# Kernel tuning notes

Measured on AMD Instinct MI355X. Metric: run time of the kernel, lower is better.

Reference implementation:

```python
import jax, jax.numpy as jnp
import numpy as np

C = 768            # config.channels
CH, CW = 16, 16    # coarse span shape for group 'screen'
N = CH * CW        # total coarse positions = 256
FH, FW, FP = 16, 16, 2
F = FH * FW * FP   # fine_total = 512
K = 4              # top4 sample mode
B = 1024           # sb


def _ln(x, g, b, eps=1e-5):
    m = jnp.mean(x, axis=-1, keepdims=True)
    v = jnp.mean((x - m) ** 2, axis=-1, keepdims=True)
    return (x - m) / jnp.sqrt(v + eps) * g + b


def _mlp3(x, W1, b1, W2, b2, W3, b3):
    h = jax.nn.gelu(x @ W1 + b1)
    h = jax.nn.gelu(h @ W2 + b2)
    return h @ W3 + b3


def setup_inputs() -> dict:
    key = jax.random.key(0)
    ks = jax.random.split(key, 16)

    def w(k, fan_in, shape):
        return jax.random.normal(k, shape, jnp.float32) * (1.0 / np.sqrt(fan_in))

    return {
        "x": jax.random.normal(ks[0], (B, C), jnp.float32),
        "g_in": jnp.ones((C,), jnp.float32),
        "b_in": jnp.zeros((C,), jnp.float32),
        # coarse head: C -> C -> C -> N
        "cW1": w(ks[1], C, (C, C)), "cb1": jnp.zeros((C,), jnp.float32),
        "cW2": w(ks[2], C, (C, C)), "cb2": jnp.zeros((C,), jnp.float32),
        "cW3": w(ks[3], C, (C, N)), "cb3": jnp.zeros((N,), jnp.float32),
        # coarse embedding
        "emb": jax.random.normal(ks[4], (N, C), jnp.float32),
        "g_e": jnp.ones((C,), jnp.float32),
        "b_e": jnp.zeros((C,), jnp.float32),
        # fine head: 2C -> C -> C -> F
        "fW1": w(ks[5], 2 * C, (2 * C, C)), "fb1": jnp.zeros((C,), jnp.float32),
        "fW2": w(ks[6], C, (C, C)), "fb2": jnp.zeros((C,), jnp.float32),
        "fW3": w(ks[7], C, (C, F)), "fb3": jnp.zeros((F,), jnp.float32),
        # no-op head
        "nW": w(ks[8], C, (C, 1)), "nb": jnp.zeros((1,), jnp.float32),
    }


def reference(x, g_in, b_in, cW1, cb1, cW2, cb2, cW3, cb3, emb, g_e, b_e,
              fW1, fb1, fW2, fb2, fW3, fb3, nW, nb):
    b = x.shape[0]
    xn = _ln(x, g_in, b_in)                                   # (b, C)
    no_op = xn @ nW + nb                                      # (b, 1)
    coarse = _mlp3(xn, cW1, cb1, cW2, cb2, cW3, cb3)          # (b, N)

    # top4 routing
    _, i = jax.lax.top_k(coarse, K)                           # (b, K) int32
    e = _ln(emb[i], g_e, b_e)                                 # (b, K, C)
    fine_in = jnp.concatenate(
        [jnp.broadcast_to(xn[:, None, :], (b, K, C)), e], axis=-1)  # (b, K, 2C)
    fine = _mlp3(fine_in, fW1, fb1, fW2, fb2, fW3, fb3)       # (b, K, F)

    log_f = jnp.log(jnp.float32(F))
    xfull = jnp.broadcast_to(coarse[:, :, None], (b, N, F)) - log_f  # (b, N, F)
    upd = fine + log_f - jax.nn.logsumexp(fine, axis=-1, keepdims=True)
    xfull = xfull.at[jnp.arange(b)[:, None], i].add(upd)      # scatter-combine

    # per-group permute: (b, ch, cw, fh, fw, fp) -> (b, ch, fh, cw, fw, fp)
    xg = xfull.reshape(b, CH, CW, FH, FW, FP)
    xg = jnp.transpose(xg, (0, 1, 3, 2, 4, 5)).reshape(b, -1)
    return jnp.concatenate([no_op, xg], axis=-1)              # (b, 1 + N*F)
```

## Files before the change

### kernel.cpp

```cpp
#include <hip/hip_runtime.h>
#include <hip/hip_bf16.h>
#include <math.h>

typedef unsigned short u16;
typedef unsigned int   u32;
typedef __attribute__((ext_vector_type(8))) short s16x8;
typedef __attribute__((ext_vector_type(4))) float f32x4;

#define CB 768
#define NB 256
#define FB 512
#define BATCH 1024
#define OUTC 131073
#define LOGF 6.2383246250395077f

__device__ __forceinline__ u16 f2bf(float f){
    u32 u = __float_as_uint(f);
    u32 r = u + 0x7FFFu + ((u >> 16) & 1u);
    return (u16)(r >> 16);
}
__device__ __forceinline__ float bf2f(u16 s){ return __uint_as_float(((u32)s) << 16); }
__device__ __forceinline__ bool probe_bf(const void* g){ return ((const u16*)g)[0] == 0x3F80u; }
__device__ __forceinline__ float loadraw(const void* p, size_t i, bool isbf){
    return isbf ? bf2f(((const u16*)p)[i]) : ((const float*)p)[i];
}
__device__ __forceinline__ void split3(float f, u16& h, u16& l, u16& q){
    h = f2bf(f); float r1 = f - bf2f(h);
    l = f2bf(r1); float r2 = r1 - bf2f(l);
    q = f2bf(r2);
}
__device__ __forceinline__ float gelu_f(float x){
    return 0.5f * x * (1.0f + tanhf(0.7978845608028654f * (x + 0.044715f * x * x * x)));
}
__device__ __forceinline__ f32x4 mfma16x16x32(s16x8 a, s16x8 b, f32x4 c){
    return __builtin_amdgcn_mfma_f32_16x16x32_bf16(a, b, c, 0, 0, 0);
}

__device__ __forceinline__ float blockReduce(float v, float* sb, bool domax){
    #pragma unroll
    for (int o = 32; o > 0; o >>= 1){
        float ov = __shfl_down(v, o, 64);
        v = domax ? fmaxf(v, ov) : (v + ov);
    }
    int w = threadIdx.x >> 6, lane = threadIdx.x & 63;
    if (lane == 0) sb[w] = v;
    __syncthreads();
    float r = domax ? fmaxf(fmaxf(sb[0], sb[1]), fmaxf(sb[2], sb[3]))
                    : (sb[0] + sb[1] + sb[2] + sb[3]);
    __syncthreads();
    return r;
}

struct TransDesc { const void* src; u16* dh; u16* dl; int K; int N; int start; int tilesX; };
struct TD6 { TransDesc d[6]; };

#define T_TRANS   3456
#define T_LNX_END 4480
#define T_LEM_END 4736
#define T_CI_END  4752
#define T_KS_END  4768
#define T_GRID    4769

__global__ __launch_bounds__(256) void prep_k(TD6 td,
        const void* x, const void* g, const void* bb, const void* nW, const void* nb,
        const void* emb, const void* ge, const void* be, const void* cb3, const void* ginp,
        u16* __restrict__ xh, u16* __restrict__ xl, u16* __restrict__ xq,
        u16* __restrict__ lnemb, float* __restrict__ noop,
        float* __restrict__ coarse, unsigned char* __restrict__ ksel,
        float* __restrict__ sumexp){
    __shared__ float t[32][33];
    __shared__ float sb[4];
    bool isbf = probe_bf(ginp);
    int blk = blockIdx.x, tid = threadIdx.x;
    if (blk < T_TRANS){
        int e = 0;
        #pragma unroll
        for (int i = 1; i < 6; i++) if (blk >= td.d[i].start) e = i;
        TransDesc d = td.d[e];
        int rel = blk - d.start;
        int n0 = (rel % d.tilesX) * 32;
        int k0 = (rel / d.tilesX) * 32;
        int tx = tid & 31, ty = tid >> 5;
        #pragma unroll
        for (int i = 0; i < 32; i += 8)
            t[ty + i][tx] = loadraw(d.src, (size_t)(k0 + ty + i) * d.N + n0 + tx, isbf);
        __syncthreads();
        #pragma unroll
        for (int i = 0; i < 32; i += 8){
            float f = t[tx][ty + i];
            u16 h = f2bf(f);
            d.dh[(size_t)(n0 + ty + i) * d.K + k0 + tx] = h;
            if (d.dl)
                d.dl[(size_t)(n0 + ty + i) * d.K + k0 + tx] = f2bf(f - bf2f(h));
        }
    } else if (blk < T_LNX_END){
        int b = blk - T_TRANS;
        float v[3];
        #pragma unroll
        for (int i = 0; i < 3; i++) v[i] = loadraw(x, (size_t)b * CB + tid + i * 256, isbf);
        float mean = blockReduce(v[0] + v[1] + v[2], sb, false) * (1.0f / 768.0f);
        float d0 = v[0] - mean, d1 = v[1] - mean, d2 = v[2] - mean;
        float var = blockReduce(d0*d0 + d1*d1 + d2*d2, sb, false) * (1.0f / 768.0f);
        float inv = 1.0f / sqrtf(var + 1e-5f);
        float dot = 0.0f;
        #pragma unroll
        for (int i = 0; i < 3; i++){
            int c = tid + i * 256;
            float xi = (v[i] - mean) * inv * loadraw(g, c, isbf) + loadraw(bb, c, isbf);
            u16 h, l, q; split3(xi, h, l, q);
            size_t o = (size_t)b * CB + c;
            xh[o] = h; xl[o] = l; xq[o] = q;
            dot += xi * loadraw(nW, c, isbf);
        }
        dot = blockReduce(dot, sb, false);
        if (tid == 0) noop[b] = dot + loadraw(nb, 0, isbf);
    } else if (blk < T_LEM_END){
        int n = blk - T_LNX_END;
        float v[3];
        #pragma unroll
        for (int i = 0; i < 3; i++) v[i] = loadraw(emb, (size_t)n * CB + tid + i * 256, isbf);
        float mean = blockReduce(v[0] + v[1] + v[2], sb, false) * (1.0f / 768.0f);
        float d0 = v[0] - mean, d1 = v[1] - mean, d2 = v[2] - mean;
        float var = blockReduce(d0*d0 + d1*d1 + d2*d2, sb, false) * (1.0f / 768.0f);
        float inv = 1.0f / sqrtf(var + 1e-5f);
        #pragma unroll
        for (int i = 0; i < 3; i++){
            int c = tid + i * 256;
            lnemb[(size_t)n * CB + c] =
                f2bf((v[i] - mean) * inv * loadraw(ge, c, isbf) + loadraw(be, c, isbf));
        }
    } else if (blk < T_CI_END){
        int base = (blk - T_LEM_END) * 16384;
        #pragma unroll
        for (int j = 0; j < 64; j++){
            int i = base + j * 256 + tid;
            coarse[i] = loadraw(cb3, i & 255, isbf);
        }
    } else if (blk < T_KS_END){
        int base = (blk - T_CI_END) * 4096;
        u32* kp = (u32*)ksel;
        #pragma unroll
        for (int j = 0; j < 16; j++) kp[base + j * 256 + tid] = 0xFFFFFFFFu;
    } else {
        #pragma unroll
        for (int j = 0; j < 16; j++) sumexp[j * 256 + tid] = 0.0f;
    }
}

template<int ASPLIT, int BSPLIT, int ACT, int OUTMODE, int TM, int TN, int GATHER>
__device__ __forceinline__ void gemm_body(u16* sm,
        const u16* __restrict__ Ah, const u16* __restrict__ Al, const u16* __restrict__ Aq,
        const int* __restrict__ gidx,
        const u16* __restrict__ Bth, const u16* __restrict__ Btl,
        const void* __restrict__ bias, bool isbf,
        void* __restrict__ o0, void* __restrict__ o1, void* __restrict__ o2,
        int bx, int by, int kbeg, int kend, int N, int lda, int ldb){
    constexpr int LDA = 72;
    constexpr int MT = TM / 32;
    constexpr int NT = TN / 64;
    constexpr int AC = TM / 64;
    constexpr int BC = TN / 64;
    u16* As = sm;
    u16* Bs = sm + ASPLIT * TM * LDA;
    const int m0 = by * TM, n0 = bx * TN;
    const int tid = threadIdx.x;
    const int w = tid >> 6, lane = tid & 63, lm = lane & 15, q = lane >> 4;
    const int wr = w & 1, wc = w >> 1;
    f32x4 acc[MT][NT];
    #pragma unroll
    for (int i = 0; i < MT; i++)
        #pragma unroll
        for (int j = 0; j < NT; j++) acc[i][j] = (f32x4)(0.0f);
    const int ar = (AC == 2) ? (tid >> 2) : (tid >> 3);
    const int ac = (AC == 2) ? ((tid & 3) * 16) : ((tid & 7) * 8);
    const int bn = (BC == 2) ? (tid >> 2) : (tid >> 3);
    const int bc = (BC == 2) ? ((tid & 3) * 16) : ((tid & 7) * 8);
    const u16* Apl[3] = { Ah, Al, Aq };
    const u16* Bpl[2] = { Bth, Btl };
    const int arow = GATHER ? gidx[m0 + ar] : (m0 + ar);

    s16x8 pa[ASPLIT][AC], pb[BSPLIT][BC];
    auto load_regs = [&](int kk){
        #pragma unroll
        for (int s = 0; s < ASPLIT; s++){
            const u16* sp = Apl[s] + (size_t)arow * lda + kk + ac;
            pa[s][0] = *(const s16x8*)(sp);
            if (AC == 2) pa[s][1] = *(const s16x8*)(sp + 8);
        }
        #pragma unroll
        for (int s = 0; s < BSPLIT; s++){
            const u16* sp = Bpl[s] + (size_t)(n0 + bn) * ldb + kk + bc;
            pb[s][0] = *(const s16x8*)(sp);
            if (BC == 2) pb[s][1] = *(const s16x8*)(sp + 8);
        }
    };

    load_regs(kbeg);
    for (int k0 = kbeg; k0 < kend; k0 += 64){
        __syncthreads();
        #pragma unroll
        for (int s = 0; s < ASPLIT; s++){
            *(s16x8*)&As[s*TM*LDA + ar*LDA + ac] = pa[s][0];
            if (AC == 2) *(s16x8*)&As[s*TM*LDA + ar*LDA + ac + 8] = pa[s][1];
        }
        #pragma unroll
        for (int s = 0; s < BSPLIT; s++){
            *(s16x8*)&Bs[s*TN*LDA + bn*LDA + bc] = pb[s][0];
            if (BC == 2) *(s16x8*)&Bs[s*TN*LDA + bn*LDA + bc + 8] = pb[s][1];
        }
        __syncthreads();
        if (k0 + 64 < kend) load_regs(k0 + 64);

        #pragma unroll
        for (int kk = 0; kk < 2; kk++){
            s16x8 afr[ASPLIT][MT], bfr[BSPLIT][NT];
            #pragma unroll
            for (int mt = 0; mt < MT; mt++)
                #pragma unroll
                for (int s = 0; s < ASPLIT; s++)
                    afr[s][mt] = *(const s16x8*)&As[s*TM*LDA + ((mt*2 + wr)*16 + lm)*LDA + kk*32 + q*8];
            #pragma unroll
            for (int nt = 0; nt < NT; nt++)
                #pragma unroll
                for (int s = 0; s < BSPLIT; s++)
                    bfr[s][nt] = *(const s16x8*)&Bs[s*TN*LDA + ((nt*4 + wc)*16 + lm)*LDA + kk*32 + q*8];
            #pragma unroll
            for (int mt = 0; mt < MT; mt++)
                #pragma unroll
                for (int nt = 0; nt < NT; nt++){
                    acc[mt][nt] = mfma16x16x32(afr[0][mt], bfr[0][nt], acc[mt][nt]);
                    if (ASPLIT == 3){
                        acc[mt][nt] = mfma16x16x32(afr[1][mt], bfr[0][nt], acc[mt][nt]);
                        acc[mt][nt] = mfma16x16x32(afr[2][mt], bfr[0][nt], acc[mt][nt]);
                    }
                    if (BSPLIT == 2){
                        acc[mt][nt] = mfma16x16x32(afr[0][mt], bfr[1][nt], acc[mt][nt]);
                        if (ASPLIT == 3)
                            acc[mt][nt] = mfma16x16x32(afr[1][mt], bfr[1][nt], acc[mt][nt]);
                    }
                }
        }
    }

    if (OUTMODE == 3){
        #pragma unroll
        for (int nt = 0; nt < NT; nt++){
            int n = n0 + (nt*4 + wc)*16 + lm;
            #pragma unroll
            for (int mt = 0; mt < MT; mt++)
                #pragma unroll
                for (int r = 0; r < 4; r++){
                    int m = m0 + (mt*2 + wr)*16 + q*4 + r;
                    atomicAdd(&((float*)o0)[(size_t)m * N + n], acc[mt][nt][r]);
                }
        }
    } else if (OUTMODE == 4){
        #pragma unroll
        for (int mt = 0; mt < MT; mt++)
            #pragma unroll
            for (int r = 0; r < 4; r++){
                int m = m0 + (mt*2 + wr)*16 + q*4 + r;
                float esum = 0.0f;
                #pragma unroll
                for (int nt = 0; nt < NT; nt++){
                    int n = n0 + (nt*4 + wc)*16 + lm;
                    float vv = acc[mt][nt][r] + (bias ? loadraw(bias, n, isbf) : 0.0f);
                    ((float*)o0)[(size_t)m * N + n] = vv;
                    esum += expf(vv);
                }
                #pragma unroll
                for (int o = 8; o > 0; o >>= 1) esum += __shfl_down(esum, o, 16);
                if (lm == 0) atomicAdd(&((float*)o1)[m], esum);
            }
    } else if (OUTMODE == 5){
        #pragma unroll
        for (int nt = 0; nt < NT; nt++){
            int n = n0 + (nt*4 + wc)*16 + lm;
            float bv = bias ? loadraw(bias, n, isbf) : 0.0f;
            #pragma unroll
            for (int mt = 0; mt < MT; mt++){
                #pragma unroll
                for (int r = 0; r < 4; r++){
                    int m = m0 + (mt*2 + wr)*16 + q*4 + r;
                    float xv = ((const float*)o1)[(size_t)(m >> 2) * N + n];
                    ((u16*)o0)[(size_t)m * N + n] = f2bf(gelu_f(acc[mt][nt][r] + bv + xv));
                }
            }
        }
    } else {
        #pragma unroll
        for (int nt = 0; nt < NT; nt++){
            int n = n0 + (nt*4 + wc)*16 + lm;
            float bv = bias ? loadraw(bias, n, isbf) : 0.0f;
            #pragma unroll
            for (int mt = 0; mt < MT; mt++){
                #pragma unroll
                for (int r = 0; r < 4; r++){
                    int m = m0 + (mt*2 + wr)*16 + q*4 + r;
                    float vv = acc[mt][nt][r] + bv;
                    if (ACT == 1) vv = gelu_f(vv);
                    size_t o = (size_t)m * N + n;
                    if (OUTMODE == 0)      ((float*)o0)[o] = vv;
                    else if (OUTMODE == 1) ((u16*)o0)[o] = f2bf(vv);
                    else {
                        u16 h, l, qq; split3(vv, h, l, qq);
                        ((u16*)o0)[o] = h; ((u16*)o1)[o] = l; ((u16*)o2)[o] = qq;
                    }
                }
            }
        }
    }
}

template<int ASPLIT, int BSPLIT, int ACT, int OUTMODE, int TM, int TN, int GATHER, int MINW>
__global__ __launch_bounds__(512, MINW) void gemm_k(
        const u16* __restrict__ Ah, const u16* __restrict__ Al, const u16* __restrict__ Aq,
        const int* __restrict__ gidx,
        const u16* __restrict__ Bth, const u16* __restrict__ Btl,
        const void* __restrict__ bias, const void* __restrict__ ginp,
        void* __restrict__ o0, void* __restrict__ o1, void* __restrict__ o2,
        int K, int N, int lda, int ldb){
    __shared__ u16 sm[(ASPLIT * TM + BSPLIT * TN) * 72];
    bool isbf = probe_bf(ginp);
    const int kc = K / gridDim.z;
    const int kbeg = blockIdx.z * kc;
    gemm_body<ASPLIT, BSPLIT, ACT, OUTMODE, TM, TN, GATHER>(sm,
        Ah, Al, Aq, gidx, Bth, Btl, bias, isbf, o0, o1, o2,
        blockIdx.x, blockIdx.y, kbeg, kbeg + kc, N, lda, ldb);
}

__global__ __launch_bounds__(512, 2) void c1x_k(
        const u16* __restrict__ xh, const u16* __restrict__ xl, const u16* __restrict__ xq,
        const u16* __restrict__ cW1th, const u16* __restrict__ cW1tl,
        const void* __restrict__ cb1, const void* __restrict__ ginp,
        u16* __restrict__ h1h, u16* __restrict__ h1l, u16* __restrict__ h1q,
        const u16* __restrict__ fW1t, float* __restrict__ xpart){
    __shared__ u16 sm[(3 * 64 + 2 * 64) * 72];
    bool isbf = probe_bf(ginp);
    if (blockIdx.x < 192){
        gemm_body<3, 2, 1, 2, 64, 64, 0>(sm, xh, xl, xq, nullptr, cW1th, cW1tl,
            cb1, isbf, h1h, h1l, h1q, blockIdx.x % 12, blockIdx.x / 12, 0, 768,
            768, 768, 768);
    } else {
        int rel = blockIdx.x - 192;
        gemm_body<1, 1, 0, 0, 128, 128, 0>(sm, xh, nullptr, nullptr, nullptr, fW1t, nullptr,
            nullptr, isbf, xpart, nullptr, nullptr, rel % 6, rel / 6, 0, 768,
            768, 768, 1536);
    }
}

__global__ __launch_bounds__(256) void topk_k(const float* __restrict__ coarse,
        int* __restrict__ idx, unsigned char* __restrict__ ksel){
    int w = threadIdx.x >> 6, lane = threadIdx.x & 63;
    int b = blockIdx.x * 4 + w;
    const float* cr = coarse + (size_t)b * NB;
    float v[4]; int id[4];
    #pragma unroll
    for (int j = 0; j < 4; j++){ id[j] = lane + 64*j; v[j] = cr[id[j]]; }
    for (int k = 0; k < 4; k++){
        float bv = v[0]; int bi = id[0];
        #pragma unroll
        for (int j = 1; j < 4; j++)
            if (v[j] > bv || (v[j] == bv && id[j] < bi)){ bv = v[j]; bi = id[j]; }
        #pragma unroll
        for (int o = 32; o > 0; o >>= 1){
            float ov = __shfl_xor(bv, o, 64);
            int   oi = __shfl_xor(bi, o, 64);
            if (ov > bv || (ov == bv && oi < bi)){ bv = ov; bi = oi; }
        }
        if (lane == 0){ idx[b*4 + k] = bi; ksel[(size_t)b * NB + bi] = (unsigned char)k; }
        #pragma unroll
        for (int j = 0; j < 4; j++) if (id[j] == bi) v[j] = -INFINITY;
    }
}

__global__ __launch_bounds__(256) void out_k(const float* __restrict__ coarse,
        const float* __restrict__ fine, const float* __restrict__ sumexp,
        const unsigned char* __restrict__ ksel, const float* __restrict__ noop,
        const void* __restrict__ ginp, void* __restrict__ outp){
    u32 g0 = ((u32)blockIdx.x * 256u + (u32)threadIdx.x) * 8u;
    const u32 total = (u32)BATCH * (u32)OUTC;
    if (g0 >= total) return;
    bool isbf = probe_bf(ginp);
    u32 qq = g0 >> 17;
    int rr = (int)(g0 & 131071u) - (int)qq;
    if (rr < 0){ qq -= 1u; rr += 131073; }
    int b = (int)qq;
    int lastkey = -1, ks = 255, fr = 0;
    float cv = 0.0f, lbase = 0.0f;
    float vals[8];
    #pragma unroll
    for (int e = 0; e < 8; e++){
        float val;
        if (rr == 0){
            val = noop[b];
        } else {
            int j = rr - 1;
            int n = ((j >> 13) << 4) | ((j >> 5) & 15);
            int key = (b << 8) | n;
            if (key != lastkey){
                lastkey = key;
                size_t o = (size_t)b * NB + n;
                cv = coarse[o] - LOGF;
                ks = ksel[o];
                if (ks != 255){
                    fr = b * 4 + ks;
                    lbase = LOGF - logf(sumexp[fr]);
                }
            }
            val = cv;
            if (ks != 255)
                val += fine[((size_t)fr << 9) + (((j >> 9) & 15) << 5) + (j & 31)] + lbase;
        }
        vals[e] = val;
        rr++;
        if (rr == 131073){ rr = 0; b++; }
    }
    if (isbf){
        u16 res[8];
        #pragma unroll
        for (int e = 0; e < 8; e++) res[e] = f2bf(vals[e]);
        *(s16x8*)((u16*)outp + g0) = *(s16x8*)res;
    } else {
        float* of = (float*)outp + g0;
        *(float4*)(of)     = make_float4(vals[0], vals[1], vals[2], vals[3]);
        *(float4*)(of + 4) = make_float4(vals[4], vals[5], vals[6], vals[7]);
    }
}

extern "C" void kernel_launch(void* const* d_in, const int* in_sizes, int n_in,
                              void* d_out, int out_size, void* d_ws, size_t ws_size,
                              hipStream_t stream){
    (void)in_sizes; (void)n_in; (void)out_size; (void)ws_size;
    char* ws = (char*)d_ws;
    size_t off = 0;
    auto alloc = [&](size_t bytes){ void* p = ws + off; off += (bytes + 255) & ~(size_t)255; return p; };

    u16* xh  = (u16*)alloc((size_t)1024*768*2);
    u16* xl  = (u16*)alloc((size_t)1024*768*2);
    u16* xq  = (u16*)alloc((size_t)1024*768*2);
    u16* h1h = (u16*)alloc((size_t)1024*768*2);
    u16* h1l = (u16*)alloc((size_t)1024*768*2);
    u16* h1q = (u16*)alloc((size_t)1024*768*2);
    u16* h2h = (u16*)alloc((size_t)1024*768*2);
    u16* h2l = (u16*)alloc((size_t)1024*768*2);
    u16* h2q = (u16*)alloc((size_t)1024*768*2);
    u16* lnemb = (u16*)alloc((size_t)256*768*2);
    float* coarse = (float*)alloc((size_t)1024*256*4);
    unsigned char* ksel = (unsigned char*)alloc((size_t)1024*256);
    float* noop   = (float*)alloc((size_t)1024*4);
    float* sumexp = (float*)alloc((size_t)4096*4);
    int*   idx    = (int*)alloc((size_t)4096*4);
    float* xpart  = (float*)alloc((size_t)1024*768*4);
    u16*   gg1    = (u16*)  alloc((size_t)4096*768*2);
    u16*   gg2    = (u16*)  alloc((size_t)4096*768*2);
    float* fine   = (float*)alloc((size_t)4096*512*4);
    u16* cW1th = (u16*)alloc((size_t)768*768*2);
    u16* cW1tl = (u16*)alloc((size_t)768*768*2);
    u16* cW2th = (u16*)alloc((size_t)768*768*2);
    u16* cW2tl = (u16*)alloc((size_t)768*768*2);
    u16* cW3th = (u16*)alloc((size_t)768*256*2);
    u16* cW3tl = (u16*)alloc((size_t)768*256*2);
    u16* fW1t  = (u16*)alloc((size_t)768*1536*2);
    u16* fW2t  = (u16*)alloc((size_t)768*768*2);
    u16* fW3t  = (u16*)alloc((size_t)512*768*2);

    const void* ginp = d_in[1];

    TD6 td;
    td.d[0] = { d_in[3],  cW1th, cW1tl,  768, 768,    0, 24 };
    td.d[1] = { d_in[5],  cW2th, cW2tl,  768, 768,  576, 24 };
    td.d[2] = { d_in[7],  cW3th, cW3tl,  768, 256, 1152,  8 };
    td.d[3] = { d_in[12], fW1t,  nullptr,1536, 768, 1344, 24 };
    td.d[4] = { d_in[14], fW2t,  nullptr, 768, 768, 2496, 24 };
    td.d[5] = { d_in[16], fW3t,  nullptr, 768, 512, 3072, 16 };

    prep_k<<<T_GRID, 256, 0, stream>>>(td, d_in[0], d_in[1], d_in[2], d_in[18], d_in[19],
            d_in[9], d_in[10], d_in[11], d_in[8], ginp,
            xh, xl, xq, lnemb, noop, coarse, ksel, sumexp);

    c1x_k<<<dim3(240, 1, 1), 512, 0, stream>>>(
            xh, xl, xq, cW1th, cW1tl, d_in[4], ginp, h1h, h1l, h1q, fW1t, xpart);

    gemm_k<3,2,1,2,64,64,0,2><<<dim3(12, 16, 1), 512, 0, stream>>>(
            h1h, h1l, h1q, nullptr, cW2th, cW2tl,
            d_in[6], ginp, h2h, h2l, h2q, 768, 768, 768, 768);
    gemm_k<3,2,0,3,64,64,0,2><<<dim3(4, 16, 4), 512, 0, stream>>>(
            h2h, h2l, h2q, nullptr, cW3th, cW3tl,
            nullptr, ginp, coarse, nullptr, nullptr, 768, 256, 768, 768);

    topk_k<<<256, 256, 0, stream>>>(coarse, idx, ksel);

    gemm_k<1,1,0,5,64,128,1,4><<<dim3(6, 64, 1), 512, 0, stream>>>(
            lnemb, nullptr, nullptr, idx, fW1t + 768, nullptr,
            d_in[13], ginp, gg1, xpart, nullptr, 768, 768, 768, 1536);
    gemm_k<1,1,1,1,64,128,0,4><<<dim3(6, 64, 1), 512, 0, stream>>>(
            gg1, nullptr, nullptr, nullptr, fW2t, nullptr,
            d_in[15], ginp, gg2, nullptr, nullptr, 768, 768, 768, 768);
    gemm_k<1,1,0,4,64,128,0,4><<<dim3(4, 64, 1), 512, 0, stream>>>(
            gg2, nullptr, nullptr, nullptr, fW3t, nullptr,
            d_in[17], ginp, fine, sumexp, nullptr, 768, 512, 768, 768);

    u32 total_chunks = ((u32)BATCH * (u32)OUTC) / 8u;
    u32 blocks = (total_chunks + 255u) / 256u;
    out_k<<<blocks, 256, 0, stream>>>(coarse, fine, sumexp, ksel, noop, ginp, d_out);
}
```

Before: 714.5 us.

## Precompute embedding projection per coarse slot and fuse gather-add into topk

Instead of running a gathered GEMM over 4096 rows of embedding times the second half of fW1, the code precomputes the projection of all 256 normalized embeddings once, as extra blocks in the first coarse GEMM launch. The topk kernel then gathers the projected rows by index, adds xpart and the bias, applies GELU and writes gg1 directly. This removes a 4096x768x768 GEMM and one launch in exchange for a small 256-row GEMM and an elementwise gather pass. The projection is now held in an fp32 workspace and summed in a different order, so rounding may differ slightly from the old gathered GEMM.

```diff
diff --git a/kernel.cpp b/kernel.cpp
--- a/kernel.cpp
+++ b/kernel.cpp
@@ -334,25 +334,35 @@
         const u16* __restrict__ cW1th, const u16* __restrict__ cW1tl,
         const void* __restrict__ cb1, const void* __restrict__ ginp,
         u16* __restrict__ h1h, u16* __restrict__ h1l, u16* __restrict__ h1q,
-        const u16* __restrict__ fW1t, float* __restrict__ xpart){
+        const u16* __restrict__ fW1t, float* __restrict__ xpart,
+        const u16* __restrict__ lnemb, float* __restrict__ embW){
     __shared__ u16 sm[(3 * 64 + 2 * 64) * 72];
     bool isbf = probe_bf(ginp);
     if (blockIdx.x < 192){
         gemm_body<3, 2, 1, 2, 64, 64, 0>(sm, xh, xl, xq, nullptr, cW1th, cW1tl,
             cb1, isbf, h1h, h1l, h1q, blockIdx.x % 12, blockIdx.x / 12, 0, 768,
             768, 768, 768);
-    } else {
+    } else if (blockIdx.x < 240){
         int rel = blockIdx.x - 192;
         gemm_body<1, 1, 0, 0, 128, 128, 0>(sm, xh, nullptr, nullptr, nullptr, fW1t, nullptr,
             nullptr, isbf, xpart, nullptr, nullptr, rel % 6, rel / 6, 0, 768,
             768, 768, 1536);
-    }
-}
-
-__global__ __launch_bounds__(256) void topk_k(const float* __restrict__ coarse,
-        int* __restrict__ idx, unsigned char* __restrict__ ksel){
+    } else {
+        int rel = blockIdx.x - 240;
+        gemm_body<1, 1, 0, 0, 128, 128, 0>(sm, lnemb, nullptr, nullptr, nullptr, fW1t + 768, nullptr,
+            nullptr, isbf, embW, nullptr, nullptr, rel % 6, rel / 6, 0, 768,
+            768, 768, 1536);
+    }
+}
+
+__global__ __launch_bounds__(512) void topk_fadd_k(const float* __restrict__ coarse,
+        unsigned char* __restrict__ ksel,
+        const float* __restrict__ embW, const float* __restrict__ xpart,
+        const void* __restrict__ fb1, const void* __restrict__ ginp,
+        u16* __restrict__ gg1){
+    __shared__ int idx_s[32];
     int w = threadIdx.x >> 6, lane = threadIdx.x & 63;
-    int b = blockIdx.x * 4 + w;
+    int b = blockIdx.x * 8 + w;
     const float* cr = coarse + (size_t)b * NB;
     float v[4]; int id[4];
     #pragma unroll
@@ -368,9 +378,37 @@
             int   oi = __shfl_xor(bi, o, 64);
             if (ov > bv || (ov == bv && oi < bi)){ bv = ov; bi = oi; }
         }
-        if (lane == 0){ idx[b*4 + k] = bi; ksel[(size_t)b * NB + bi] = (unsigned char)k; }
+        if (lane == 0){
+            idx_s[w*4 + k] = bi;
+            ksel[(size_t)b * NB + bi] = (unsigned char)k;
+        }
         #pragma unroll
         for (int j = 0; j < 4; j++) if (id[j] == bi) v[j] = -INFINITY;
+    }
+    __syncthreads();
+    bool isbf = probe_bf(ginp);
+    int fr0 = blockIdx.x * 32;
+    #pragma unroll
+    for (int j = 0; j < 6; j++){
+        int c = (int)threadIdx.x + j * 512;
+        int r = c / 96;
+        int col = (c - r * 96) * 8;
+        int fr = fr0 + r;
+        int bb2 = fr >> 2;
+        int n = idx_s[r];
+        const float* ew = embW + (size_t)n * CB + col;
+        const float* xr = xpart + (size_t)bb2 * CB + col;
+        float4 e0 = *(const float4*)ew, e1 = *(const float4*)(ew + 4);
+        float4 x0 = *(const float4*)xr, x1 = *(const float4*)(xr + 4);
+        float ev[8] = {e0.x,e0.y,e0.z,e0.w,e1.x,e1.y,e1.z,e1.w};
+        float xv[8] = {x0.x,x0.y,x0.z,x0.w,x1.x,x1.y,x1.z,x1.w};
+        u16 res[8];
+        #pragma unroll
+        for (int e = 0; e < 8; e++){
+            float bv = loadraw(fb1, col + e, isbf);
+            res[e] = f2bf(gelu_f((ev[e] + bv) + xv[e]));
+        }
+        *(s16x8*)(gg1 + (size_t)fr * CB + col) = *(s16x8*)res;
     }
 }
 
@@ -450,7 +488,7 @@
     unsigned char* ksel = (unsigned char*)alloc((size_t)1024*256);
     float* noop   = (float*)alloc((size_t)1024*4);
     float* sumexp = (float*)alloc((size_t)4096*4);
-    int*   idx    = (int*)alloc((size_t)4096*4);
+    float* embW   = (float*)alloc((size_t)256*768*4);
     float* xpart  = (float*)alloc((size_t)1024*768*4);
     u16*   gg1    = (u16*)  alloc((size_t)4096*768*2);
     u16*   gg2    = (u16*)  alloc((size_t)4096*768*2);
@@ -479,8 +517,9 @@
             d_in[9], d_in[10], d_in[11], d_in[8], ginp,
             xh, xl, xq, lnemb, noop, coarse, ksel, sumexp);
 
-    c1x_k<<<dim3(240, 1, 1), 512, 0, stream>>>(
-            xh, xl, xq, cW1th, cW1tl, d_in[4], ginp, h1h, h1l, h1q, fW1t, xpart);
+    c1x_k<<<dim3(252, 1, 1), 512, 0, stream>>>(
+            xh, xl, xq, cW1th, cW1tl, d_in[4], ginp, h1h, h1l, h1q,
+            fW1t, xpart, lnemb, embW);
 
     gemm_k<3,2,1,2,64,64,0,2><<<dim3(12, 16, 1), 512, 0, stream>>>(
             h1h, h1l, h1q, nullptr, cW2th, cW2tl,
@@ -489,11 +528,8 @@
             h2h, h2l, h2q, nullptr, cW3th, cW3tl,
             nullptr, ginp, coarse, nullptr, nullptr, 768, 256, 768, 768);
 
-    topk_k<<<256, 256, 0, stream>>>(coarse, idx, ksel);
-
-    gemm_k<1,1,0,5,64,128,1,4><<<dim3(6, 64, 1), 512, 0, stream>>>(
-            lnemb, nullptr, nullptr, idx, fW1t + 768, nullptr,
-            d_in[13], ginp, gg1, xpart, nullptr, 768, 768, 768, 1536);
+    topk_fadd_k<<<128, 512, 0, stream>>>(coarse, ksel, embW, xpart, d_in[13], ginp, gg1);
+
     gemm_k<1,1,1,1,64,128,0,4><<<dim3(6, 64, 1), 512, 0, stream>>>(
             gg1, nullptr, nullptr, nullptr, fW2t, nullptr,
             d_in[15], ginp, gg2, nullptr, nullptr, 768, 768, 768, 768);
```

Result: no change. 714.9 us (+0.0%).
